# Performance work log

Measured on AMD Instinct MI355X. Metric: run time of the kernel, lower is better.

## Reference

```python
import jax, jax.numpy as jnp
import numpy as np
from jax import lax

OUT_SIZE = 224  # original input spatial size (output_size of anomaly map)
NUM_NEIGHBORS = 9
SIGMA = 4.0
KSIZE = 2 * int(4.0 * SIGMA + 0.5) + 1  # 33, kornia-style kernel size


def avg_pool3(x):
    # AvgPool2d(3, 1, 1), count_include_pad=True -> sum over 3x3 window / 9
    s = lax.reduce_window(x, 0.0, lax.add, (1, 1, 3, 3), (1, 1, 1, 1),
                          [(0, 0), (0, 0), (1, 1), (1, 1)])
    return s / 9.0


def euclidean_dist(x, y):
    # x: [..., N, E], y: [..., M, E] -> [..., N, M]
    x_norm = jnp.sum(x * x, axis=-1, keepdims=True)
    y_norm = jnp.sum(y * y, axis=-1, keepdims=True)
    res = x_norm - 2.0 * jnp.matmul(x, jnp.swapaxes(y, -2, -1)) + jnp.swapaxes(y_norm, -2, -1)
    return jnp.sqrt(jnp.clip(res, 0.0))


def gaussian_blur(x):
    # x: [B,1,H,W]; separable Gaussian, reflect padding (kornia GaussianBlur2d default)
    r = KSIZE // 2
    t = jnp.arange(KSIZE, dtype=x.dtype) - r
    k = jnp.exp(-(t * t) / (2.0 * SIGMA * SIGMA))
    k = k / jnp.sum(k)
    xp = jnp.pad(x, ((0, 0), (0, 0), (r, r), (r, r)), mode='reflect')
    kh = k.reshape(1, 1, KSIZE, 1)
    kw = k.reshape(1, 1, 1, KSIZE)
    y = lax.conv_general_dilated(xp, kh, (1, 1), 'VALID',
                                 dimension_numbers=('NCHW', 'OIHW', 'NCHW'))
    return lax.conv_general_dilated(y, kw, (1, 1), 'VALID',
                                    dimension_numbers=('NCHW', 'OIHW', 'NCHW'))


def compute_anomaly_score(patch_scores, locations, embedding, memory_bank):
    # patch_scores/locations: [B, P]; embedding: [B*P, E]; memory_bank: [M, E]
    batch, num_patches = patch_scores.shape
    bidx = jnp.arange(batch)
    max_patches = jnp.argmax(patch_scores, axis=1)                       # [B]
    max_feats = embedding.reshape(batch, num_patches, -1)[bidx, max_patches]  # [B,E]
    score = patch_scores[bidx, max_patches]                              # [B]
    nn_index = locations[bidx, max_patches]                              # [B]
    nn_sample = memory_bank[nn_index]                                    # [B,E]
    n_nb = min(NUM_NEIGHBORS, memory_bank.shape[0])
    d_bank = euclidean_dist(nn_sample, memory_bank)                      # [B,M]
    _, support = lax.top_k(-d_bank, n_nb)                                # [B,k] smallest
    sup_feats = memory_bank[support]                                     # [B,k,E]
    d = euclidean_dist(max_feats[:, None, :], sup_feats)[:, 0, :]        # [B,k]
    weights = (1.0 - jax.nn.softmax(d, axis=1))[:, 0]                    # [B]
    return weights * score


def setup_inputs() -> dict:
    key = jax.random.key(0)
    k1, k2, k3 = jax.random.split(key, 3)
    feat2 = jax.random.normal(k1, (8, 512, 28, 28), dtype=jnp.float32)
    feat3 = jax.random.normal(k2, (8, 1024, 14, 14), dtype=jnp.float32)
    memory_bank = jax.random.normal(k3, (20000, 1536), dtype=jnp.float32)
    return {'feat2': feat2, 'feat3': feat3, 'memory_bank': memory_bank}


def reference(feat2, feat3, memory_bank):
    # feature pooling (AvgPool2d(3,1,1) on each backbone layer)
    f2 = avg_pool3(feat2)
    f3 = avg_pool3(feat3)
    batch, _, height, width = f2.shape
    # generate_embedding: bilinear upsample deeper layer, concat along channels
    f3u = jax.image.resize(f3, (batch, f3.shape[1], height, width), method='bilinear')
    emb = jnp.concatenate([f2, f3u], axis=1)                 # [B,1536,28,28]
    emb_dim = emb.shape[1]
    embedding = emb.transpose(0, 2, 3, 1).reshape(-1, emb_dim)  # [B*784, 1536]
    # nearest_neighbors with n_neighbors=1
    dist = euclidean_dist(embedding, memory_bank)            # [N, M]
    patch_scores = jnp.min(dist, axis=1)
    locations = jnp.argmin(dist, axis=1)
    patch_scores = patch_scores.reshape(batch, -1)
    locations = locations.reshape(batch, -1)
    pred_score = compute_anomaly_score(patch_scores, locations, embedding, memory_bank)
    # anomaly map: bilinear upsample patch scores to input size + gaussian blur
    score_map = patch_scores.reshape(batch, 1, width, height)
    amap = jax.image.resize(score_map, (batch, 1, OUT_SIZE, OUT_SIZE), method='bilinear')
    anomaly_map = gaussian_blur(amap)
    return anomaly_map, pred_score
```

## Files before the change

### kernel.cpp

```cpp
#include <hip/hip_runtime.h>
#include <math.h>

#define NB 8
#define C2 512
#define C3 1024
#define H2 28
#define W2 28
#define H3 14
#define W3 14
#define EDIM 1536
#define PPB (H2*W2)
#define NPATCH (NB*PPB)
#define MPAD 6400
#define MBANK 20000
#define OUTW 224
#define NNB 9
#define KS 33
#define KR 16
#define NMT 25
#define NNT 79
#define CHUNKS 8
#define CH (MBANK/CHUNKS)
#define MPB 64

#define SXQ 63.5f
#define SYQ (127.0f/6.0f)

typedef __attribute__((ext_vector_type(4))) int   i32x4;
typedef __attribute__((ext_vector_type(4))) float f32x4;

#define LEXLT(va,ia,vb,ib) ((va) < (vb) || ((va)==(vb) && (ia)<(ib)))
#define CSWAP(va,ia,vb,ib) { if (LEXLT(va,ia,vb,ib)) { float _tv=(vb); int _ti=(ib); (vb)=(va); (ib)=(ia); (va)=_tv; (ia)=_ti; } }

#define BAR() asm volatile("s_barrier" ::: "memory")
#define WAITV4() asm volatile("s_waitcnt vmcnt(4)" ::: "memory")
#define WAITV0() asm volatile("s_waitcnt vmcnt(0)" ::: "memory")

__device__ __forceinline__ void gload16(const void* g, void* l) {
  __builtin_amdgcn_global_load_lds(
      (const __attribute__((address_space(1))) unsigned int*)g,
      (__attribute__((address_space(3))) unsigned int*)l, 16, 0, 0);
}
__device__ __forceinline__ signed char q8(float x, float s) {
  int v = (int)rintf(x * s);
  v = v > 127 ? 127 : (v < -127 ? -127 : v);
  return (signed char)v;
}


__global__ __launch_bounds__(256) void pool2_kernel(const float* __restrict__ in,
    float* __restrict__ emb32, signed char* __restrict__ embq) {
  int bid = blockIdx.x;
  int cg = bid & 7; int h = (bid >> 3) % H2; int b = bid / (8*H2);
  int t = threadIdx.x;
  __shared__ float s3[3][64][29];
  for (int li = t; li < 3*64*28; li += 256) {
    int w = li % 28; int c = (li/28) & 63; int dh = li/(28*64);
    int hh = h + dh - 1;
    float v = 0.f;
    if (hh >= 0 && hh < H2) v = in[((size_t)(b*C2) + cg*64 + c)*784 + hh*28 + w];
    s3[dh][c][w] = v;
  }
  __syncthreads();
  for (int o = t; o < 64*28; o += 256) {
    int c = o & 63, w = o >> 6;
    float s = 0.f;
    #pragma unroll
    for (int dh = 0; dh < 3; ++dh) {
      s += s3[dh][c][w];
      if (w > 0)  s += s3[dh][c][w-1];
      if (w < 27) s += s3[dh][c][w+1];
    }
    s *= (1.f/9.f);
    size_t idx = ((size_t)(b*PPB) + h*28 + w)*EDIM + cg*64 + c;
    emb32[idx] = s;
    embq[idx] = q8(s, SXQ);
  }
}

__global__ void pool3_kernel(const float* __restrict__ in, float* __restrict__ f3p) {
  int id = blockIdx.x*blockDim.x + threadIdx.x;
  if (id >= NB*C3*H3*W3) return;
  int w = id % W3, h = (id / W3) % H3, c = (id / (H3*W3)) % C3, b = id / (C3*H3*W3);
  const float* src = in + (size_t)(b*C3 + c)*H3*W3;
  float s = 0.f;
  #pragma unroll
  for (int dh=-1; dh<=1; ++dh) {
    int hh = h+dh; if (hh<0||hh>=H3) continue;
    #pragma unroll
    for (int dw=-1; dw<=1; ++dw) {
      int ww = w+dw; if (ww<0||ww>=W3) continue;
      s += src[hh*W3+ww];
    }
  }
  f3p[(size_t)id] = s * (1.f/9.f);
}

__global__ __launch_bounds__(256) void up3_kernel(const float* __restrict__ f3p,
    float* __restrict__ emb32, signed char* __restrict__ embq) {
  int bid = blockIdx.x;
  int cg = bid & 15; int i = (bid >> 4) % H2; int b = bid / (16*H2);
  int t = threadIdx.x;
  float sy = i*0.5f - 0.25f; sy = fminf(fmaxf(sy,0.f),(float)(H3-1));
  int y0 = (int)sy; int y1 = min(y0+1,H3-1); float fy = sy - (float)y0;
  __shared__ float r2[2][64][15];
  for (int li = t; li < 2*64*14; li += 256) {
    int w = li % 14; int c = (li/14) & 63; int yy = li/(14*64);
    int ysrc = yy ? y1 : y0;
    r2[yy][c][w] = f3p[((size_t)(b*C3) + cg*64 + c)*196 + ysrc*14 + w];
  }
  __syncthreads();
  for (int o = t; o < 64*28; o += 256) {
    int c = o & 63, j = o >> 6;
    float sx = j*0.5f - 0.25f; sx = fminf(fmaxf(sx,0.f),(float)(W3-1));
    int x0 = (int)sx; int x1 = min(x0+1,W3-1); float fx = sx - (float)x0;
    float v = (1.f-fy)*((1.f-fx)*r2[0][c][x0] + fx*r2[0][c][x1])
            +      fy *((1.f-fx)*r2[1][c][x0] + fx*r2[1][c][x1]);
    size_t idx = ((size_t)(b*PPB) + i*28 + j)*EDIM + C2 + cg*64 + c;
    emb32[idx] = v;
    embq[idx] = q8(v, SXQ);
  }
}


__global__ void bank_prep_kernel(const float* __restrict__ bank, signed char* __restrict__ bankq,
                                 float* __restrict__ yn) {
  int w = (blockIdx.x*blockDim.x + threadIdx.x) >> 6;
  int lane = threadIdx.x & 63;
  if (w >= MBANK) return;
  const float4* p = reinterpret_cast<const float4*>(bank + (size_t)w*EDIM);
  int* q = reinterpret_cast<int*>(bankq + (size_t)w*EDIM);
  float acc = 0.f;
  #pragma unroll
  for (int k = 0; k < EDIM/4/64; ++k) {
    int k4 = lane + k*64;
    float4 v = p[k4];
    acc = fmaf(v.x,v.x,acc); acc = fmaf(v.y,v.y,acc);
    acc = fmaf(v.z,v.z,acc); acc = fmaf(v.w,v.w,acc);
    unsigned pk = ((unsigned)(unsigned char)q8(v.x, SYQ))
                | ((unsigned)(unsigned char)q8(v.y, SYQ) << 8)
                | ((unsigned)(unsigned char)q8(v.z, SYQ) << 16)
                | ((unsigned)(unsigned char)q8(v.w, SYQ) << 24);
    q[k4] = (int)pk;
  }
  #pragma unroll
  for (int s = 32; s; s >>= 1) acc += __shfl_xor(acc, s);
  if (lane == 0) yn[w] = acc;
}

__global__ void norm32_kernel(const float* __restrict__ src, float* __restrict__ norms, int rows) {
  int w = (blockIdx.x*blockDim.x + threadIdx.x) >> 6;
  int lane = threadIdx.x & 63;
  if (w >= rows) return;
  const float4* p = reinterpret_cast<const float4*>(src + (size_t)w*EDIM);
  float acc = 0.f;
  for (int k = lane; k < EDIM/4; k += 64) {
    float4 v = p[k];
    acc = fmaf(v.x,v.x,acc); acc = fmaf(v.y,v.y,acc);
    acc = fmaf(v.z,v.z,acc); acc = fmaf(v.w,v.w,acc);
  }
  #pragma unroll
  for (int s = 32; s; s >>= 1) acc += __shfl_xor(acc, s);
  if (lane == 0) norms[w] = acc;
}


__global__ __launch_bounds__(512, 2) void dist_min_i8(
    const signed char* __restrict__ A, const signed char* __restrict__ B,
    const float* __restrict__ yn, float* __restrict__ outq, int* __restrict__ outi)
{
  __shared__ __align__(16) unsigned char LDSC[131072];
  const int t = threadIdx.x;
  const int lane = t & 63, wid = t >> 6;
  const int wr = wid >> 2, wc = wid & 3;

  const int nwg = NMT*NNT;
  int orig = blockIdx.x;
  int xcd = orig & 7, loc = orig >> 3;
  int qq = nwg >> 3, rm = nwg & 7;
  int wg = (xcd < rm ? xcd*(qq+1) : rm*(qq+1) + (xcd-rm)*qq) + loc;
  const int mt = wg / NNT, nt = wg % NNT;
  const int m0 = mt*256, n0 = nt*256;

  const int l3 = lane >> 3, l7 = lane & 7;
  const int D = l7 ^ l3;
  const int koS = (D & 3) << 4;
  const int rhi = D >> 2;
  const int r0 = wid*32 + (l3<<1) + rhi;
  const int r1 = r0 + 16;
  const char* Ac = (const char*)A + (size_t)m0*EDIM;
  const char* Bc = (const char*)B;
  const unsigned aoff0 = (unsigned)(r0*EDIM + koS);
  const unsigned aoff1 = (unsigned)(r1*EDIM + koS);
  int bn0 = n0 + r0; bn0 = bn0 < MBANK ? bn0 : MBANK-1;
  int bn1 = n0 + r1; bn1 = bn1 < MBANK ? bn1 : MBANK-1;
  const unsigned boff0 = (unsigned)bn0*(unsigned)EDIM + (unsigned)koS;
  const unsigned boff1 = (unsigned)bn1*(unsigned)EDIM + (unsigned)koS;
  char* const dstBase = (char*)LDSC + (wid << 11);

  const int h = lane & 15, g = lane >> 4;
  const int csw = (((h & 1) << 2) | g) ^ (h >> 1);
  const unsigned abyte = (unsigned)(((wr*128 + h) >> 1)*128 + csw*16);
  const unsigned bbyte = (unsigned)(((wc*64 + h) >> 1)*128 + csw*16);

  i32x4 acc[8][4];
  #pragma unroll
  for (int i = 0; i < 8; ++i)
    #pragma unroll
    for (int j = 0; j < 4; ++j) acc[i][j] = (i32x4){0,0,0,0};
  i32x4 bfv[4];

  #pragma unroll
  for (int s = 0; s < 3; ++s) {
    const unsigned sl = (unsigned)s*16384u;
    gload16(Ac + aoff0 + s*64, dstBase + sl);
    gload16(Ac + aoff1 + s*64, dstBase + sl + 1024);
    gload16(Bc + boff0 + s*64, dstBase + 65536u + sl);
    gload16(Bc + boff1 + s*64, dstBase + 65536u + sl + 1024);
  }
  WAITV4();
  BAR();

  for (int it = 0; it < 6; ++it) {
    const int sb = it << 2;
    #pragma unroll
    for (int ph = 0; ph < 8; ++ph) {
      const int cs = sb + (ph >> 1);
      const unsigned sA = (unsigned)(cs & 3)*16384u;
      i32x4 af[4];
      if ((ph & 1) == 0) {
        const unsigned sB = sA + 65536u;
        #pragma unroll
        for (int j = 0; j < 4; ++j)
          bfv[j] = *(const i32x4*)(LDSC + sB + bbyte + j*1024);
        #pragma unroll
        for (int i = 0; i < 4; ++i)
          af[i] = *(const i32x4*)(LDSC + sA + abyte + i*1024);
      } else {
        #pragma unroll
        for (int i = 0; i < 4; ++i)
          af[i] = *(const i32x4*)(LDSC + sA + abyte + (i+4)*1024);
      }
      int ss = sb + 3 + (ph >> 1); ss = ss < 24 ? ss : 23;
      const unsigned dsl = (unsigned)(ss & 3)*16384u + ((ph & 1) ? 65536u : 0u);
      if (ph & 1) {
        gload16(Bc + boff0 + ss*64, dstBase + dsl);
        gload16(Bc + boff1 + ss*64, dstBase + dsl + 1024);
      } else {
        gload16(Ac + aoff0 + ss*64, dstBase + dsl);
        gload16(Ac + aoff1 + ss*64, dstBase + dsl + 1024);
      }
      BAR();
      __builtin_amdgcn_s_setprio(1);
      const int fb = (ph & 1) << 2;
      #pragma unroll
      for (int i = 0; i < 4; ++i)
        #pragma unroll
        for (int j = 0; j < 4; ++j)
          acc[fb+i][j] = __builtin_amdgcn_mfma_i32_16x16x64_i8(af[i], bfv[j], acc[fb+i][j], 0, 0, 0);
      __builtin_amdgcn_s_setprio(0);
      if (ph == 3 || ph == 7) WAITV4();
      BAR();
    }
  }
  WAITV0();
  BAR();

  const float NEG2INV = -2.0f * (2.0f/127.0f) * (6.0f/127.0f);
  float ynv[4];
  #pragma unroll
  for (int j = 0; j < 4; ++j) {
    int col = n0 + wc*64 + j*16 + h;
    ynv[j] = col < MBANK ? yn[col] : INFINITY;
  }
  float* smin = (float*)LDSC;
  int* sidx = (int*)(LDSC + 4096);
  #pragma unroll
  for (int i = 0; i < 8; ++i) {
    #pragma unroll
    for (int r = 0; r < 4; ++r) {
      float v = INFINITY; int ix = 0x7fffffff;
      #pragma unroll
      for (int j = 0; j < 4; ++j) {
        float q = fmaf(NEG2INV, (float)acc[i][j][r], ynv[j]);
        int col = n0 + wc*64 + j*16 + h;
        if (q < v || (q == v && col < ix)) { v = q; ix = col; }
      }
      #pragma unroll
      for (int m = 1; m < 16; m <<= 1) {
        float ov = __shfl_xor(v, m);
        int   oi = __shfl_xor(ix, m);
        if (ov < v || (ov == v && oi < ix)) { v = ov; ix = oi; }
      }
      if (h == 0) {
        int rl = wr*128 + i*16 + g*4 + r;
        smin[rl*4 + wc] = v;
        sidx[rl*4 + wc] = ix;
      }
    }
  }
  __syncthreads();
  if (t < 256) {
    float v = smin[t*4]; int ix = sidx[t*4];
    #pragma unroll
    for (int w = 1; w < 4; ++w) {
      float ov = smin[t*4+w]; int oi = sidx[t*4+w];
      if (ov < v || (ov == v && oi < ix)) { v = ov; ix = oi; }
    }
    int row = m0 + t;
    if (row < NPATCH) {
      outq[(size_t)nt*NPATCH + row] = v;
      outi[(size_t)nt*NPATCH + row] = ix;
    }
  }
}

__global__ void reduce_min_kernel(const float* __restrict__ outq, const int* __restrict__ outi,
                                  int* __restrict__ loc) {
  int r = blockIdx.x*blockDim.x + threadIdx.x;
  if (r >= NPATCH) return;
  float bv = INFINITY; int bi = 0x7fffffff;
  for (int s = 0; s < NNT; ++s) {
    float v = outq[(size_t)s*NPATCH + r];
    int  ix = outi[(size_t)s*NPATCH + r];
    if (v < bv || (v == bv && ix < bi)) { bv = v; bi = ix; }
  }
  loc[r] = bi;
}

__global__ void rescore_kernel(const float* __restrict__ emb32, const float* __restrict__ bank,
                               const float* __restrict__ xn, const float* __restrict__ yn,
                               const int* __restrict__ loc, float* __restrict__ ps) {
  int w = (blockIdx.x*blockDim.x + threadIdx.x) >> 6;
  int lane = threadIdx.x & 63;
  if (w >= NPATCH) return;
  int j = loc[w];
  const float4* x = reinterpret_cast<const float4*>(emb32 + (size_t)w*EDIM);
  const float4* y = reinterpret_cast<const float4*>(bank + (size_t)j*EDIM);
  float acc = 0.f;
  #pragma unroll
  for (int k = 0; k < EDIM/4/64; ++k) {
    float4 a = x[lane + k*64], b = y[lane + k*64];
    acc = fmaf(a.x,b.x,acc); acc = fmaf(a.y,b.y,acc);
    acc = fmaf(a.z,b.z,acc); acc = fmaf(a.w,b.w,acc);
  }
  #pragma unroll
  for (int s = 32; s; s >>= 1) acc += __shfl_xor(acc, s);
  if (lane == 0) ps[w] = sqrtf(fmaxf(xn[w] - 2.f*acc + yn[j], 0.f));
}


__global__ void argmax_kernel(const float* __restrict__ ps, const int* __restrict__ loc,
                              float* __restrict__ bscore, int* __restrict__ brow, int* __restrict__ bnn) {
  __shared__ float sv[256]; __shared__ int si[256];
  int b = blockIdx.x, t = threadIdx.x;
  float bv = -INFINITY; int bi = 0x7fffffff;
  for (int p = t; p < PPB; p += 256) {
    float v = ps[b*PPB + p];
    if (v > bv || (v == bv && p < bi)) { bv = v; bi = p; }
  }
  sv[t] = bv; si[t] = bi; __syncthreads();
  for (int s = 128; s; s >>= 1) {
    if (t < s) {
      if (sv[t+s] > sv[t] || (sv[t+s] == sv[t] && si[t+s] < si[t])) { sv[t] = sv[t+s]; si[t] = si[t+s]; }
    }
    __syncthreads();
  }
  if (t == 0) {
    bscore[b] = sv[0];
    brow[b]   = b*PPB + si[0];
    bnn[b]    = loc[b*PPB + si[0]];
  }
}

__global__ __launch_bounds__(256) void dbank_kernel(
    const float* __restrict__ bank, const float* __restrict__ yn,
    const int* __restrict__ bnn, float* __restrict__ dbank)
{
  __shared__ float xs[8][EDIM];
  int t = threadIdx.x;
  for (int idx = t*4; idx < 8*EDIM; idx += 256*4) {
    int b = idx / EDIM, k = idx % EDIM;
    float4 v = *reinterpret_cast<const float4*>(bank + (size_t)bnn[b]*EDIM + k);
    *reinterpret_cast<float4*>(&xs[b][k]) = v;
  }
  __syncthreads();
  int lane = t & 63, w = t >> 6;
  for (int u = 0; u < MPB/4; ++u) {
    int m = blockIdx.x*MPB + u*4 + w;
    if (m < MBANK) {
      const float4* yp = reinterpret_cast<const float4*>(bank + (size_t)m*EDIM);
      float acc[8] = {0.f,0.f,0.f,0.f,0.f,0.f,0.f,0.f};
      for (int k4 = lane; k4 < EDIM/4; k4 += 64) {
        float4 y = yp[k4];
        int k = k4*4;
        #pragma unroll
        for (int b = 0; b < 8; ++b) {
          acc[b] = fmaf(y.x, xs[b][k+0], acc[b]);
          acc[b] = fmaf(y.y, xs[b][k+1], acc[b]);
          acc[b] = fmaf(y.z, xs[b][k+2], acc[b]);
          acc[b] = fmaf(y.w, xs[b][k+3], acc[b]);
        }
      }
      #pragma unroll
      for (int b = 0; b < 8; ++b) {
        float a = acc[b];
        #pragma unroll
        for (int s = 32; s; s >>= 1) a += __shfl_xor(a, s);
        acc[b] = a;
      }
      if (lane == 0) {
        #pragma unroll
        for (int b = 0; b < 8; ++b) {
          int nn = bnn[b];
          float d2 = yn[nn] - 2.f*acc[b] + yn[m];
          dbank[(size_t)b*MBANK + m] = sqrtf(fmaxf(d2, 0.f));
        }
      }
    }
  }
}


__global__ __launch_bounds__(256) void top9_stage1(const float* __restrict__ dbank,
                                                   float* __restrict__ cv, int* __restrict__ ci) {
  int b = blockIdx.x / CHUNKS, ch = blockIdx.x % CHUNKS;
  const float* db = dbank + (size_t)b*MBANK + ch*CH;
  int t = threadIdx.x;

  float v0=INFINITY,v1=INFINITY,v2=INFINITY,v3=INFINITY,v4=INFINITY,
        v5=INFINITY,v6=INFINITY,v7=INFINITY,v8=INFINITY;
  int i0=0x7fffffff,i1=0x7fffffff,i2=0x7fffffff,i3=0x7fffffff,i4=0x7fffffff,
      i5=0x7fffffff,i6=0x7fffffff,i7=0x7fffffff,i8=0x7fffffff;

  for (int s = 0; s < (CH+255)/256; ++s) {
    int m = t + s*256;
    if (m < CH) {
      float nv = db[m]; int ni = ch*CH + m;
      if (LEXLT(nv,ni,v8,i8)) {
        v8 = nv; i8 = ni;
        CSWAP(v8,i8,v7,i7); CSWAP(v7,i7,v6,i6); CSWAP(v6,i6,v5,i5); CSWAP(v5,i5,v4,i4);
        CSWAP(v4,i4,v3,i3); CSWAP(v3,i3,v2,i2); CSWAP(v2,i2,v1,i1); CSWAP(v1,i1,v0,i0);
      }
    }
  }

  __shared__ float sv[256*9];
  __shared__ int   si[256*9];
  __shared__ float rv[256]; __shared__ int ri[256]; __shared__ int rp[256];
  sv[t*9+0]=v0; sv[t*9+1]=v1; sv[t*9+2]=v2; sv[t*9+3]=v3; sv[t*9+4]=v4;
  sv[t*9+5]=v5; sv[t*9+6]=v6; sv[t*9+7]=v7; sv[t*9+8]=v8;
  si[t*9+0]=i0; si[t*9+1]=i1; si[t*9+2]=i2; si[t*9+3]=i3; si[t*9+4]=i4;
  si[t*9+5]=i5; si[t*9+6]=i6; si[t*9+7]=i7; si[t*9+8]=i8;
  __syncthreads();

  for (int r = 0; r < NNB; ++r) {
    float bv = INFINITY; int bix = 0x7fffffff; int bp = -1;
    #pragma unroll
    for (int u = 0; u < 9; ++u) {
      float v = sv[t*9+u]; int ix = si[t*9+u];
      if (LEXLT(v,ix,bv,bix)) { bv = v; bix = ix; bp = t*9+u; }
    }
    rv[t] = bv; ri[t] = bix; rp[t] = bp; __syncthreads();
    for (int s = 128; s; s >>= 1) {
      if (t < s) {
        if (LEXLT(rv[t+s],ri[t+s],rv[t],ri[t])) { rv[t]=rv[t+s]; ri[t]=ri[t+s]; rp[t]=rp[t+s]; }
      }
      __syncthreads();
    }
    if (t == 0) {
      cv[blockIdx.x*NNB + r] = rv[0];
      ci[blockIdx.x*NNB + r] = ri[0];
      sv[rp[0]] = INFINITY; si[rp[0]] = 0x7fffffff;
    }
    __syncthreads();
  }
}


__global__ void top9_stage2(const float* __restrict__ cv, const int* __restrict__ ci,
                            int* __restrict__ support) {
  __shared__ float sv[128]; __shared__ int si[128];
  __shared__ float wv[128]; __shared__ int wi[128]; __shared__ int wp[128];
  int b = blockIdx.x, t = threadIdx.x;
  if (t < CHUNKS*NNB) { sv[t] = cv[b*CHUNKS*NNB + t]; si[t] = ci[b*CHUNKS*NNB + t]; }
  else { sv[t] = INFINITY; si[t] = 0x7fffffff; }
  __syncthreads();
  for (int r = 0; r < NNB; ++r) {
    wv[t] = sv[t]; wi[t] = si[t]; wp[t] = t; __syncthreads();
    for (int s = 64; s; s >>= 1) {
      if (t < s) {
        if (LEXLT(wv[t+s],wi[t+s],wv[t],wi[t])) { wv[t]=wv[t+s]; wi[t]=wi[t+s]; wp[t]=wp[t+s]; }
      }
      __syncthreads();
    }
    if (t == 0) {
      support[b*NNB + r] = wi[0];
      sv[wp[0]] = INFINITY; si[wp[0]] = 0x7fffffff;
    }
    __syncthreads();
  }
}

__global__ void dsup_kernel(const float* __restrict__ emb32, const float* __restrict__ bank,
                            const float* __restrict__ xn, const float* __restrict__ yn,
                            const int* __restrict__ brow, const int* __restrict__ support,
                            float* __restrict__ dsup) {
  int w = (blockIdx.x*blockDim.x + threadIdx.x) >> 6;
  int lane = threadIdx.x & 63;
  if (w >= NB*NNB) return;
  int b = w / NNB, j = w % NNB;
  int row = brow[b]; int sup = support[b*NNB + j];
  const float* x = emb32 + (size_t)row*EDIM;
  const float* y = bank + (size_t)sup*EDIM;
  float acc = 0.f;
  for (int k = lane; k < EDIM; k += 64) acc = fmaf(x[k], y[k], acc);
  #pragma unroll
  for (int s = 32; s; s >>= 1) acc += __shfl_xor(acc, s);
  if (lane == 0) dsup[b*NNB + j] = sqrtf(fmaxf(xn[row] - 2.f*acc + yn[sup], 0.f));
}

__global__ void pred_kernel(const float* __restrict__ dsup, const float* __restrict__ bscore,
                            float* __restrict__ out) {
  int b = threadIdx.x;
  if (b >= NB) return;
  float d[NNB]; float mx = -INFINITY;
  #pragma unroll
  for (int j = 0; j < NNB; ++j) { d[j] = dsup[b*NNB + j]; mx = fmaxf(mx, d[j]); }
  float s = 0.f;
  #pragma unroll
  for (int j = 0; j < NNB; ++j) s += expf(d[j] - mx);
  float w = 1.f - expf(d[0] - mx) / s;
  out[b] = w * bscore[b];
}


__device__ __forceinline__ int refl224(int x) {
  if (x < 0) return -x;
  if (x > OUTW-1) return 2*(OUTW-1) - x;
  return x;
}

__global__ __launch_bounds__(256) void upblurh_kernel(const float* __restrict__ ps,
                                                      float* __restrict__ tmp) {
  int b = blockIdx.x / OUTW, i = blockIdx.x % OUTW;
  int t = threadIdx.x;
  __shared__ float l[W2];
  __shared__ float graw[KS];
  if (t < KS) {
    float x = (float)t - (float)KR;
    graw[t] = expf(-(x*x) / (2.f*4.f*4.f));
  }
  float sy = ((float)i + 0.5f)*0.125f - 0.5f; sy = fminf(fmaxf(sy,0.f),(float)(H2-1));
  int y0 = (int)sy; int y1 = min(y0+1,H2-1); float fy = sy - (float)y0;
  if (t < W2) {
    const float* p = ps + b*PPB;
    l[t] = (1.f-fy)*p[y0*W2+t] + fy*p[y1*W2+t];
  }
  __syncthreads();
  if (t >= OUTW) return;
  float gsum = 0.f;
  #pragma unroll
  for (int u = 0; u < KS; ++u) gsum += graw[u];
  float winv = 1.f / gsum;
  float s = 0.f;
  #pragma unroll
  for (int v = 0; v < KS; ++v) {
    int jj = refl224(t - KR + v);
    float sx = ((float)jj + 0.5f)*0.125f - 0.5f; sx = fminf(fmaxf(sx,0.f),(float)(W2-1));
    int x0 = (int)sx; int x1 = min(x0+1,W2-1); float fx = sx - (float)x0;
    s = fmaf(graw[v]*winv, (1.f-fx)*l[x0] + fx*l[x1], s);
  }
  tmp[((size_t)b*OUTW + i)*OUTW + t] = s;
}

__global__ __launch_bounds__(256) void blurv_kernel(const float* __restrict__ in,
                                                    float* __restrict__ out) {
  __shared__ float graw[KS];
  int t = threadIdx.x;
  if (t < KS) {
    float x = (float)t - (float)KR;
    graw[t] = expf(-(x*x) / (2.f*4.f*4.f));
  }
  __syncthreads();
  int id = blockIdx.x*blockDim.x + t;
  if (id >= NB*OUTW*OUTW) return;
  float gsum = 0.f;
  #pragma unroll
  for (int u = 0; u < KS; ++u) gsum += graw[u];
  float winv = 1.f / gsum;
  int j = id % OUTW, i = (id/OUTW) % OUTW, b = id/(OUTW*OUTW);
  float s = 0.f;
  #pragma unroll
  for (int u = 0; u < KS; ++u) {
    int ii = refl224(i - KR + u);
    s = fmaf(graw[u]*winv, in[((size_t)b*OUTW + ii)*OUTW + j], s);
  }
  out[id] = s;
}


extern "C" void kernel_launch(void* const* d_in, const int* in_sizes, int n_in,
                              void* d_out, int out_size, void* d_ws, size_t ws_size,
                              hipStream_t stream) {
  const float* feat2 = (const float*)d_in[0];
  const float* feat3 = (const float*)d_in[1];
  const float* bank  = (const float*)d_in[2];
  float* out = (float*)d_out;

  char* base = (char*)d_ws;
  size_t off = 0;
  auto alloc = [&](size_t nbytes) -> char* {
    char* p = base + off;
    off += ((nbytes + 255) & ~(size_t)255);
    return p;
  };
  float*       emb32 = (float*)      alloc((size_t)NPATCH*EDIM*4);
  signed char* embq  = (signed char*)alloc((size_t)MPAD*EDIM);
  signed char* bankq = (signed char*)alloc((size_t)MBANK*EDIM);
  float* f3p    = (float*)alloc((size_t)NB*C3*H3*W3*4);
  float* yn     = (float*)alloc(MBANK*4);
  float* xn     = (float*)alloc(NPATCH*4);
  float* outq   = (float*)alloc((size_t)NNT*NPATCH*4);
  int*   outi   = (int*)  alloc((size_t)NNT*NPATCH*4);
  float* ps     = (float*)alloc(NPATCH*4);
  int*   loc    = (int*)  alloc(NPATCH*4);
  float* bscore = (float*)alloc(NB*4);
  int*   brow   = (int*)  alloc(NB*4);
  int*   bnn    = (int*)  alloc(NB*4);
  float* dbank  = (float*)alloc((size_t)NB*MBANK*4);
  float* cv     = (float*)alloc(NB*CHUNKS*NNB*4);
  int*   ci     = (int*)  alloc(NB*CHUNKS*NNB*4);
  int*   supp   = (int*)  alloc(NB*NNB*4);
  float* dsup   = (float*)alloc(NB*NNB*4);
  float* tmp    = (float*)alloc((size_t)NB*OUTW*OUTW*4);

  pool2_kernel<<<NB*H2*8, 256, 0, stream>>>(feat2, emb32, embq);
  {
    int n = NB*C3*H3*W3;
    pool3_kernel<<<(n+255)/256, 256, 0, stream>>>(feat3, f3p);
  }
  up3_kernel<<<NB*H2*16, 256, 0, stream>>>(f3p, emb32, embq);
  bank_prep_kernel<<<(MBANK*64)/256, 256, 0, stream>>>(bank, bankq, yn);
  norm32_kernel<<<(NPATCH*64+255)/256, 256, 0, stream>>>(emb32, xn, NPATCH);

  dist_min_i8<<<NMT*NNT, 512, 0, stream>>>(embq, bankq, yn, outq, outi);
  reduce_min_kernel<<<(NPATCH+255)/256, 256, 0, stream>>>(outq, outi, loc);
  rescore_kernel<<<(NPATCH*64)/256, 256, 0, stream>>>(emb32, bank, xn, yn, loc, ps);

  argmax_kernel<<<NB, 256, 0, stream>>>(ps, loc, bscore, brow, bnn);
  dbank_kernel<<<(MBANK+MPB-1)/MPB, 256, 0, stream>>>(bank, yn, bnn, dbank);
  top9_stage1<<<NB*CHUNKS, 256, 0, stream>>>(dbank, cv, ci);
  top9_stage2<<<NB, 128, 0, stream>>>(cv, ci, supp);
  dsup_kernel<<<(NB*NNB*64 + 255)/256, 256, 0, stream>>>(emb32, bank, xn, yn, brow, supp, dsup);
  pred_kernel<<<1, 64, 0, stream>>>(dsup, bscore, out + NB*OUTW*OUTW);

  {
    upblurh_kernel<<<NB*OUTW, 256, 0, stream>>>(ps, tmp);
    int n = NB*OUTW*OUTW;
    blurv_kernel<<<(n+255)/256, 256, 0, stream>>>(tmp, out);
  }
}
```

Before: 538.7 us.

## Restructure int8 GEMM main loop, fold norms into rescore, quantize dbank

```diff
diff --git a/kernel.cpp b/kernel.cpp
--- a/kernel.cpp
+++ b/kernel.cpp
@@ -22,6 +22,7 @@
 #define CHUNKS 8
 #define CH (MBANK/CHUNKS)
 #define MPB 64
+#define NSLAB 24
 
 #define SXQ 63.5f
 #define SYQ (127.0f/6.0f)
@@ -33,6 +34,7 @@
 #define CSWAP(va,ia,vb,ib) { if (LEXLT(va,ia,vb,ib)) { float _tv=(vb); int _ti=(ib); (vb)=(va); (ib)=(ia); (va)=_tv; (ia)=_ti; } }
 
 #define BAR() asm volatile("s_barrier" ::: "memory")
+#define WAITV8() asm volatile("s_waitcnt vmcnt(8)" ::: "memory")
 #define WAITV4() asm volatile("s_waitcnt vmcnt(4)" ::: "memory")
 #define WAITV0() asm volatile("s_waitcnt vmcnt(0)" ::: "memory")
 
@@ -146,22 +148,6 @@
   #pragma unroll
   for (int s = 32; s; s >>= 1) acc += __shfl_xor(acc, s);
   if (lane == 0) yn[w] = acc;
-}
-
-__global__ void norm32_kernel(const float* __restrict__ src, float* __restrict__ norms, int rows) {
-  int w = (blockIdx.x*blockDim.x + threadIdx.x) >> 6;
-  int lane = threadIdx.x & 63;
-  if (w >= rows) return;
-  const float4* p = reinterpret_cast<const float4*>(src + (size_t)w*EDIM);
-  float acc = 0.f;
-  for (int k = lane; k < EDIM/4; k += 64) {
-    float4 v = p[k];
-    acc = fmaf(v.x,v.x,acc); acc = fmaf(v.y,v.y,acc);
-    acc = fmaf(v.z,v.z,acc); acc = fmaf(v.w,v.w,acc);
-  }
-  #pragma unroll
-  for (int s = 32; s; s >>= 1) acc += __shfl_xor(acc, s);
-  if (lane == 0) norms[w] = acc;
 }
 
 
@@ -208,7 +194,6 @@
   for (int i = 0; i < 8; ++i)
     #pragma unroll
     for (int j = 0; j < 4; ++j) acc[i][j] = (i32x4){0,0,0,0};
-  i32x4 bfv[4];
 
   #pragma unroll
   for (int s = 0; s < 3; ++s) {
@@ -218,53 +203,39 @@
     gload16(Bc + boff0 + s*64, dstBase + 65536u + sl);
     gload16(Bc + boff1 + s*64, dstBase + 65536u + sl + 1024);
   }
-  WAITV4();
+  WAITV8();
   BAR();
 
-  for (int it = 0; it < 6; ++it) {
-    const int sb = it << 2;
-    #pragma unroll
-    for (int ph = 0; ph < 8; ++ph) {
-      const int cs = sb + (ph >> 1);
-      const unsigned sA = (unsigned)(cs & 3)*16384u;
-      i32x4 af[4];
-      if ((ph & 1) == 0) {
-        const unsigned sB = sA + 65536u;
-        #pragma unroll
-        for (int j = 0; j < 4; ++j)
-          bfv[j] = *(const i32x4*)(LDSC + sB + bbyte + j*1024);
-        #pragma unroll
-        for (int i = 0; i < 4; ++i)
-          af[i] = *(const i32x4*)(LDSC + sA + abyte + i*1024);
-      } else {
-        #pragma unroll
-        for (int i = 0; i < 4; ++i)
-          af[i] = *(const i32x4*)(LDSC + sA + abyte + (i+4)*1024);
-      }
-      int ss = sb + 3 + (ph >> 1); ss = ss < 24 ? ss : 23;
-      const unsigned dsl = (unsigned)(ss & 3)*16384u + ((ph & 1) ? 65536u : 0u);
-      if (ph & 1) {
-        gload16(Bc + boff0 + ss*64, dstBase + dsl);
-        gload16(Bc + boff1 + ss*64, dstBase + dsl + 1024);
-      } else {
-        gload16(Ac + aoff0 + ss*64, dstBase + dsl);
-        gload16(Ac + aoff1 + ss*64, dstBase + dsl + 1024);
-      }
-      BAR();
-      __builtin_amdgcn_s_setprio(1);
-      const int fb = (ph & 1) << 2;
+  #pragma unroll 4
+  for (int p = 0; p < NSLAB; ++p) {
+    const unsigned sA = (unsigned)(p & 3)*16384u;
+    const unsigned sB = sA + 65536u;
+    i32x4 af[8], bfv[4];
+    #pragma unroll
+    for (int j = 0; j < 4; ++j)
+      bfv[j] = *(const i32x4*)(LDSC + sB + bbyte + j*1024);
+    #pragma unroll
+    for (int i = 0; i < 8; ++i)
+      af[i] = *(const i32x4*)(LDSC + sA + abyte + i*1024);
+    if (p < NSLAB-3) {
+      const unsigned sW = (unsigned)((p+3) & 3)*16384u;
+      gload16(Ac + aoff0 + (p+3)*64, dstBase + sW);
+      gload16(Ac + aoff1 + (p+3)*64, dstBase + sW + 1024);
+      gload16(Bc + boff0 + (p+3)*64, dstBase + 65536u + sW);
+      gload16(Bc + boff1 + (p+3)*64, dstBase + 65536u + sW + 1024);
+    }
+    __builtin_amdgcn_s_setprio(1);
+    #pragma unroll
+    for (int i = 0; i < 8; ++i)
       #pragma unroll
-      for (int i = 0; i < 4; ++i)
-        #pragma unroll
-        for (int j = 0; j < 4; ++j)
-          acc[fb+i][j] = __builtin_amdgcn_mfma_i32_16x16x64_i8(af[i], bfv[j], acc[fb+i][j], 0, 0, 0);
-      __builtin_amdgcn_s_setprio(0);
-      if (ph == 3 || ph == 7) WAITV4();
-      BAR();
-    }
-  }
-  WAITV0();
-  BAR();
+      for (int j = 0; j < 4; ++j)
+        acc[i][j] = __builtin_amdgcn_mfma_i32_16x16x64_i8(af[i], bfv[j], acc[i][j], 0, 0, 0);
+    __builtin_amdgcn_s_setprio(0);
+    if (p < NSLAB-3) { WAITV8(); }
+    else if (p == NSLAB-3) { WAITV4(); }
+    else if (p == NSLAB-2) { WAITV0(); }
+    BAR();
+  }
 
   const float NEG2INV = -2.0f * (2.0f/127.0f) * (6.0f/127.0f);
   float ynv[4];
@@ -329,7 +300,7 @@
 }
 
 __global__ void rescore_kernel(const float* __restrict__ emb32, const float* __restrict__ bank,
-                               const float* __restrict__ xn, const float* __restrict__ yn,
+                               const float* __restrict__ yn,
                                const int* __restrict__ loc, float* __restrict__ ps) {
   int w = (blockIdx.x*blockDim.x + threadIdx.x) >> 6;
   int lane = threadIdx.x & 63;
@@ -337,16 +308,18 @@
   int j = loc[w];
   const float4* x = reinterpret_cast<const float4*>(emb32 + (size_t)w*EDIM);
   const float4* y = reinterpret_cast<const float4*>(bank + (size_t)j*EDIM);
-  float acc = 0.f;
+  float accd = 0.f, accx = 0.f;
   #pragma unroll
   for (int k = 0; k < EDIM/4/64; ++k) {
     float4 a = x[lane + k*64], b = y[lane + k*64];
-    acc = fmaf(a.x,b.x,acc); acc = fmaf(a.y,b.y,acc);
-    acc = fmaf(a.z,b.z,acc); acc = fmaf(a.w,b.w,acc);
-  }
-  #pragma unroll
-  for (int s = 32; s; s >>= 1) acc += __shfl_xor(acc, s);
-  if (lane == 0) ps[w] = sqrtf(fmaxf(xn[w] - 2.f*acc + yn[j], 0.f));
+    accd = fmaf(a.x,b.x,accd); accd = fmaf(a.y,b.y,accd);
+    accd = fmaf(a.z,b.z,accd); accd = fmaf(a.w,b.w,accd);
+    accx = fmaf(a.x,a.x,accx); accx = fmaf(a.y,a.y,accx);
+    accx = fmaf(a.z,a.z,accx); accx = fmaf(a.w,a.w,accx);
+  }
+  #pragma unroll
+  for (int s = 32; s; s >>= 1) { accd += __shfl_xor(accd, s); accx += __shfl_xor(accx, s); }
+  if (lane == 0) ps[w] = sqrtf(fmaxf(accx - 2.f*accd + yn[j], 0.f));
 }
 
 
@@ -374,32 +347,36 @@
 }
 
 __global__ __launch_bounds__(256) void dbank_kernel(
-    const float* __restrict__ bank, const float* __restrict__ yn,
+    const signed char* __restrict__ bankq, const float* __restrict__ yn,
     const int* __restrict__ bnn, float* __restrict__ dbank)
 {
   __shared__ float xs[8][EDIM];
   int t = threadIdx.x;
-  for (int idx = t*4; idx < 8*EDIM; idx += 256*4) {
+  for (int idx = t*16; idx < 8*EDIM; idx += 256*16) {
     int b = idx / EDIM, k = idx % EDIM;
-    float4 v = *reinterpret_cast<const float4*>(bank + (size_t)bnn[b]*EDIM + k);
-    *reinterpret_cast<float4*>(&xs[b][k]) = v;
-  }
-  __syncthreads();
+    int4 v = *reinterpret_cast<const int4*>(bankq + (size_t)bnn[b]*EDIM + k);
+    const signed char* pc = (const signed char*)&v;
+    #pragma unroll
+    for (int e = 0; e < 16; ++e) xs[b][k+e] = (float)pc[e];
+  }
+  __syncthreads();
+  const float INV2 = 1.0f / (SYQ*SYQ);
   int lane = t & 63, w = t >> 6;
   for (int u = 0; u < MPB/4; ++u) {
     int m = blockIdx.x*MPB + u*4 + w;
     if (m < MBANK) {
-      const float4* yp = reinterpret_cast<const float4*>(bank + (size_t)m*EDIM);
+      const int4* yp = reinterpret_cast<const int4*>(bankq + (size_t)m*EDIM);
       float acc[8] = {0.f,0.f,0.f,0.f,0.f,0.f,0.f,0.f};
-      for (int k4 = lane; k4 < EDIM/4; k4 += 64) {
-        float4 y = yp[k4];
-        int k = k4*4;
+      for (int k16 = lane; k16 < EDIM/16; k16 += 64) {
+        int4 y = yp[k16];
+        const signed char* yc = (const signed char*)&y;
+        int k = k16*16;
         #pragma unroll
         for (int b = 0; b < 8; ++b) {
-          acc[b] = fmaf(y.x, xs[b][k+0], acc[b]);
-          acc[b] = fmaf(y.y, xs[b][k+1], acc[b]);
-          acc[b] = fmaf(y.z, xs[b][k+2], acc[b]);
-          acc[b] = fmaf(y.w, xs[b][k+3], acc[b]);
+          float a = 0.f;
+          #pragma unroll
+          for (int e = 0; e < 16; ++e) a = fmaf((float)yc[e], xs[b][k+e], a);
+          acc[b] += a;
         }
       }
       #pragma unroll
@@ -413,7 +390,7 @@
         #pragma unroll
         for (int b = 0; b < 8; ++b) {
           int nn = bnn[b];
-          float d2 = yn[nn] - 2.f*acc[b] + yn[m];
+          float d2 = yn[nn] - 2.f*acc[b]*INV2 + yn[m];
           dbank[(size_t)b*MBANK + m] = sqrtf(fmaxf(d2, 0.f));
         }
       }
@@ -503,7 +480,7 @@
 }
 
 __global__ void dsup_kernel(const float* __restrict__ emb32, const float* __restrict__ bank,
-                            const float* __restrict__ xn, const float* __restrict__ yn,
+                            const float* __restrict__ yn,
                             const int* __restrict__ brow, const int* __restrict__ support,
                             float* __restrict__ dsup) {
   int w = (blockIdx.x*blockDim.x + threadIdx.x) >> 6;
@@ -513,11 +490,15 @@
   int row = brow[b]; int sup = support[b*NNB + j];
   const float* x = emb32 + (size_t)row*EDIM;
   const float* y = bank + (size_t)sup*EDIM;
-  float acc = 0.f;
-  for (int k = lane; k < EDIM; k += 64) acc = fmaf(x[k], y[k], acc);
-  #pragma unroll
-  for (int s = 32; s; s >>= 1) acc += __shfl_xor(acc, s);
-  if (lane == 0) dsup[b*NNB + j] = sqrtf(fmaxf(xn[row] - 2.f*acc + yn[sup], 0.f));
+  float accd = 0.f, accx = 0.f;
+  for (int k = lane; k < EDIM; k += 64) {
+    float a = x[k];
+    accd = fmaf(a, y[k], accd);
+    accx = fmaf(a, a, accx);
+  }
+  #pragma unroll
+  for (int s = 32; s; s >>= 1) { accd += __shfl_xor(accd, s); accx += __shfl_xor(accx, s); }
+  if (lane == 0) dsup[b*NNB + j] = sqrtf(fmaxf(accx - 2.f*accd + yn[sup], 0.f));
 }
 
 __global__ void pred_kernel(const float* __restrict__ dsup, const float* __restrict__ bscore,
@@ -620,7 +601,6 @@
   signed char* bankq = (signed char*)alloc((size_t)MBANK*EDIM);
   float* f3p    = (float*)alloc((size_t)NB*C3*H3*W3*4);
   float* yn     = (float*)alloc(MBANK*4);
-  float* xn     = (float*)alloc(NPATCH*4);
   float* outq   = (float*)alloc((size_t)NNT*NPATCH*4);
   int*   outi   = (int*)  alloc((size_t)NNT*NPATCH*4);
   float* ps     = (float*)alloc(NPATCH*4);
@@ -642,17 +622,16 @@
   }
   up3_kernel<<<NB*H2*16, 256, 0, stream>>>(f3p, emb32, embq);
   bank_prep_kernel<<<(MBANK*64)/256, 256, 0, stream>>>(bank, bankq, yn);
-  norm32_kernel<<<(NPATCH*64+255)/256, 256, 0, stream>>>(emb32, xn, NPATCH);
 
   dist_min_i8<<<NMT*NNT, 512, 0, stream>>>(embq, bankq, yn, outq, outi);
   reduce_min_kernel<<<(NPATCH+255)/256, 256, 0, stream>>>(outq, outi, loc);
-  rescore_kernel<<<(NPATCH*64)/256, 256, 0, stream>>>(emb32, bank, xn, yn, loc, ps);
+  rescore_kernel<<<(NPATCH*64)/256, 256, 0, stream>>>(emb32, bank, yn, loc, ps);
 
   argmax_kernel<<<NB, 256, 0, stream>>>(ps, loc, bscore, brow, bnn);
-  dbank_kernel<<<(MBANK+MPB-1)/MPB, 256, 0, stream>>>(bank, yn, bnn, dbank);
+  dbank_kernel<<<(MBANK+MPB-1)/MPB, 256, 0, stream>>>(bankq, yn, bnn, dbank);
   top9_stage1<<<NB*CHUNKS, 256, 0, stream>>>(dbank, cv, ci);
   top9_stage2<<<NB, 128, 0, stream>>>(cv, ci, supp);
-  dsup_kernel<<<(NB*NNB*64 + 255)/256, 256, 0, stream>>>(emb32, bank, xn, yn, brow, supp, dsup);
+  dsup_kernel<<<(NB*NNB*64 + 255)/256, 256, 0, stream>>>(emb32, bank, yn, brow, supp, dsup);
   pred_kernel<<<1, 64, 0, stream>>>(dsup, bscore, out + NB*OUTW*OUTW);
 
   {
```

Result: slower. 561.7 us (+4.3%).
